# Kernel tuning notes

Hardware: AMD Instinct MI355X
Metric: run time of the kernel (lower is better)

Reference implementation:

```python
import jax, jax.numpy as jnp
import numpy as np

EMBED_DIM = 1024
NUM_HEADS = 16
HEAD_DIM = EMBED_DIM // NUM_HEADS


def setup_inputs() -> dict:
    key = jax.random.key(0)
    ks = jax.random.split(key, 9)
    B, S, D = 2, 2048, EMBED_DIM
    scale = 1.0 / np.sqrt(D)
    x = jax.random.normal(ks[0], (B, S, D), dtype=jnp.float32)
    wq = jax.random.normal(ks[1], (D, D), dtype=jnp.float32) * scale
    bq = jax.random.normal(ks[2], (D,), dtype=jnp.float32) * 0.02
    wk = jax.random.normal(ks[3], (D, D), dtype=jnp.float32) * scale
    bk = jax.random.normal(ks[4], (D,), dtype=jnp.float32) * 0.02
    wv = jax.random.normal(ks[5], (D, D), dtype=jnp.float32) * scale
    bv = jax.random.normal(ks[6], (D,), dtype=jnp.float32) * 0.02
    wo = jax.random.normal(ks[7], (D, D), dtype=jnp.float32) * scale
    bo = jax.random.normal(ks[8], (D,), dtype=jnp.float32) * 0.02
    return {"x": x, "wq": wq, "bq": bq, "wk": wk, "bk": bk,
            "wv": wv, "bv": bv, "wo": wo, "bo": bo}


def reference(x, wq, bq, wk, bk, wv, bv, wo, bo):
    B, S, D = x.shape
    H, Hd = NUM_HEADS, HEAD_DIM
    # separate QKV linears (weights stored [in, out] so x @ w)
    q = (x @ wq + bq).reshape(B, S, H, Hd).transpose(0, 2, 1, 3)  # [B,H,S,Hd]
    k = (x @ wk + bk).reshape(B, S, H, Hd).transpose(0, 2, 1, 3)
    v = (x @ wv + bv).reshape(B, S, H, Hd).transpose(0, 2, 1, 3)
    scores = jnp.einsum('bhqd,bhkd->bhqk', q, k) / jnp.sqrt(jnp.float32(Hd))
    attn = jax.nn.softmax(scores, axis=-1)
    context = jnp.einsum('bhqk,bhkd->bhqd', attn, v)
    context = context.transpose(0, 2, 1, 3).reshape(B, S, D)
    return context @ wo + bo
```

## Files before the change

kernel.cpp:

```cpp
#include <hip/hip_runtime.h>
#include <cstdint>
#include <cstddef>


typedef float floatx4 __attribute__((ext_vector_type(4)));
typedef __bf16 bf16x8 __attribute__((ext_vector_type(8)));
union ABFrag { bf16x8 v; uint4 q; unsigned short u[8]; unsigned int w[4]; };

__device__ __forceinline__ unsigned short f2bf(float f) {
    unsigned int u = __builtin_bit_cast(unsigned int, f);
    return (unsigned short)((u + 0x7FFFu + ((u >> 16) & 1u)) >> 16);
}

__device__ __forceinline__ unsigned int pkbf(float lo, float hi) {
    unsigned int a = __builtin_bit_cast(unsigned int, hi) + 0x8000u;
    unsigned int b = __builtin_bit_cast(unsigned int, lo) + 0x8000u;
    return __builtin_amdgcn_perm(a, b, 0x07060302u);
}

#if __has_builtin(__builtin_amdgcn_exp2f)
#define EXP2F(x) __builtin_amdgcn_exp2f(x)
#else
#define EXP2F(x) exp2f(x)
#endif

__device__ __forceinline__ void glds16(const void* g, void* l) {
    __builtin_amdgcn_global_load_lds(
        (const __attribute__((address_space(1))) unsigned int*)(uintptr_t)g,
        (__attribute__((address_space(3))) unsigned int*)(unsigned int)(uintptr_t)l,
        16, 0, 0);
}

__global__ void convert_x_kernel(const float* __restrict__ x,
                                 unsigned short* __restrict__ xb) {
    int i = (blockIdx.x * 256 + threadIdx.x) * 8;
    float4 a = *(const float4*)(x + i);
    float4 b = *(const float4*)(x + i + 4);
    union { unsigned short u[8]; uint4 q; } o;
    o.u[0] = f2bf(a.x); o.u[1] = f2bf(a.y); o.u[2] = f2bf(a.z); o.u[3] = f2bf(a.w);
    o.u[4] = f2bf(b.x); o.u[5] = f2bf(b.y); o.u[6] = f2bf(b.z); o.u[7] = f2bf(b.w);
    *(uint4*)(xb + i) = o.q;
}

__global__ void convert_wT_kernel(const float* __restrict__ w0, const float* __restrict__ w1,
                                  const float* __restrict__ w2, const float* __restrict__ w3,
                                  unsigned short* __restrict__ wT) {
    __shared__ unsigned short t[32][40];
    const float* w = (blockIdx.z == 0) ? w0 : (blockIdx.z == 1) ? w1
                   : (blockIdx.z == 2) ? w2 : w3;
    unsigned short* dst = wT + (size_t)blockIdx.z * 1024 * 1024;
    const int k0 = blockIdx.x * 32, n0 = blockIdx.y * 32;
    const int tid = threadIdx.x;
    {
        int ry = tid >> 3, cx = (tid & 7) * 4;
        float4 v = *(const float4*)(w + (size_t)(k0 + ry) * 1024 + n0 + cx);
        t[cx + 0][ry] = f2bf(v.x); t[cx + 1][ry] = f2bf(v.y);
        t[cx + 2][ry] = f2bf(v.z); t[cx + 3][ry] = f2bf(v.w);
    }
    __syncthreads();
    int n = tid >> 3, kc = (tid & 7) * 4;
    *(uint2*)(dst + (size_t)(n0 + n) * 1024 + k0 + kc) = *(const uint2*)&t[n][kc];
}

template<int KIND>
__launch_bounds__(256, 2)
__global__ void gemm_kernel(const unsigned short* __restrict__ A,
                            const unsigned short* __restrict__ wT,
                            const float* __restrict__ bias0,
                            const float* __restrict__ bias1,
                            const float* __restrict__ bias2,
                            void* __restrict__ out0,
                            void* __restrict__ out1,
                            void* __restrict__ out2)
{
    constexpr int BN = (KIND == 1) ? 64 : 128;
    constexpr int NJ = BN / 32;

    __shared__ unsigned short a_s[128 * 32];
    __shared__ unsigned short b_s[BN * 32];

    const int tid  = threadIdx.x;
    const int wid  = tid >> 6;
    const int lane = tid & 63;
    const int quad = lane >> 4;
    const int l15  = lane & 15;
    const int wm   = (wid >> 1) * 64;
    const int wn   = (wid & 1) * (BN / 2);
    const int m0   = blockIdx.y * 128;
    const int n0   = blockIdx.x * BN;

    const unsigned short* Bt = (KIND == 0) ? wT + (size_t)blockIdx.z * (1024 * 1024) : wT;
    const float* bias = (KIND == 0)
        ? (blockIdx.z == 0 ? bias0 : blockIdx.z == 1 ? bias1 : bias2) : bias0;

    const int sr = lane >> 2;
    const int sc = (lane & 3) * 8;
    const unsigned short* gA = A + (size_t)(m0 + wid * 32 + sr) * 1024 + sc;
    const unsigned short* gB = (KIND == 0)
        ? Bt + (size_t)(n0 + wid * 32 + sr) * 1024 + sc
        : Bt + (size_t)(n0 + wid * 16 + sr) * 1024 + sc;
    unsigned short* lA = a_s + wid * 1024;
    unsigned short* lB = (KIND == 0) ? b_s + wid * 1024 : b_s + wid * 512;

    floatx4 acc[4][NJ];
    #pragma unroll
    for (int i = 0; i < 4; i++)
        #pragma unroll
        for (int j = 0; j < NJ; j++)
            acc[i][j] = floatx4{0.f, 0.f, 0.f, 0.f};

    for (int k0 = 0; k0 < 1024; k0 += 32) {
        __syncthreads();
        glds16(gA + k0,             lA);
        glds16(gA + k0 + 16 * 1024, lA + 512);
        if constexpr (KIND == 0) {
            glds16(gB + k0,             lB);
            glds16(gB + k0 + 16 * 1024, lB + 512);
        } else {
            glds16(gB + k0,             lB);
        }
        __syncthreads();

        ABFrag af[4], bf4[NJ];
        #pragma unroll
        for (int i = 0; i < 4; i++)
            af[i].q = *(const uint4*)(a_s + (wm + i * 16 + l15) * 32 + quad * 8);
        #pragma unroll
        for (int j = 0; j < NJ; j++)
            bf4[j].q = *(const uint4*)(b_s + (wn + j * 16 + l15) * 32 + quad * 8);
        #pragma unroll
        for (int i = 0; i < 4; i++)
            #pragma unroll
            for (int j = 0; j < NJ; j++)
                acc[i][j] = __builtin_amdgcn_mfma_f32_16x16x32_bf16(
                    af[i].v, bf4[j].v, acc[i][j], 0, 0, 0);
    }

    if constexpr (KIND == 1) {
        float* out = (float*)out0;
        #pragma unroll
        for (int j = 0; j < NJ; j++) {
            int gn = n0 + wn + j * 16 + l15;
            float bval = bias[gn];
            #pragma unroll
            for (int i = 0; i < 4; i++)
                #pragma unroll
                for (int r = 0; r < 4; r++) {
                    int gm = m0 + wm + i * 16 + quad * 4 + r;
                    out[(size_t)gm * 1024 + gn] = acc[i][j][r] + bval;
                }
        }
    } else {
        if (blockIdx.z == 0) {
            const float SCQ = 0.125f * 1.44269504088896f;
            unsigned short* out = (unsigned short*)out0;
            #pragma unroll
            for (int j = 0; j < 4; j++) {
                int gn = n0 + wn + j * 16 + l15;
                float bval = bias[gn];
                int h = gn >> 6, d = gn & 63;
                #pragma unroll
                for (int i = 0; i < 4; i++)
                    #pragma unroll
                    for (int r = 0; r < 4; r++) {
                        int gm = m0 + wm + i * 16 + quad * 4 + r;
                        int b = gm >> 11, s = gm & 2047;
                        out[(((size_t)(b * 16 + h) * 2048 + s) << 6) + d] =
                            f2bf((acc[i][j][r] + bval) * SCQ);
                    }
            }
        } else if (blockIdx.z == 1) {
            unsigned short* out = (unsigned short*)out1;
            #pragma unroll
            for (int j = 0; j < 4; j++) {
                int gn = n0 + wn + j * 16 + l15;
                float bval = bias[gn];
                int h = gn >> 6, d = gn & 63;
                int dg = d >> 3, dl = d & 7;
                #pragma unroll
                for (int i = 0; i < 4; i++)
                    #pragma unroll
                    for (int r = 0; r < 4; r++) {
                        int gm = m0 + wm + i * 16 + quad * 4 + r;
                        int b = gm >> 11, s = gm & 2047;
                        int dphys = ((dg ^ (s & 7)) << 3) | dl;
                        out[(((size_t)(b * 16 + h) * 2048 + s) << 6) + dphys] =
                            f2bf(acc[i][j][r] + bval);
                    }
            }
        } else {
            __shared__ unsigned short t_s[128][136];
            #pragma unroll
            for (int j = 0; j < 4; j++) {
                int nl = wn + j * 16 + l15;
                float bval = bias[n0 + nl];
                #pragma unroll
                for (int i = 0; i < 4; i++)
                    #pragma unroll
                    for (int r = 0; r < 4; r++)
                        t_s[nl][wm + i * 16 + quad * 4 + r] = f2bf(acc[i][j][r] + bval);
            }
            __syncthreads();
            unsigned short* out = (unsigned short*)out2;
            const int n  = tid >> 1, half = tid & 1;
            const int bh = (m0 >> 11) * 16 + ((n0 + n) >> 6);
            const int d  = (n0 + n) & 63;
            const int chunk = ((m0 & 2047) >> 6) + half;
            const int dmask = d & 7;
            unsigned short* dstb = out + ((size_t)(bh * 32 + chunk) * 64 + d) * 64;
            const unsigned short* src = &t_s[n][half * 64];
            #pragma unroll
            for (int gp = 0; gp < 8; gp++) {
                int u1 = 32 * (gp >> 2) + 4 * (gp & 3);
                uint2 lo = *(const uint2*)(src + u1);
                uint2 hi = *(const uint2*)(src + u1 + 16);
                unsigned short* dq = dstb + ((gp ^ dmask) << 3);
                *(uint2*)dq       = lo;
                *(uint2*)(dq + 4) = hi;
            }
        }
    }
}

__launch_bounds__(512, 4)
__global__ void attn_kernel(const unsigned short* __restrict__ Q,
                            const unsigned short* __restrict__ K,
                            const unsigned short* __restrict__ Vt,
                            unsigned short* __restrict__ ctx)
{
    __shared__ unsigned short smem[2][2][2][4096];

    const int tid  = threadIdx.x;
    const int wid  = tid >> 6;
    const int kh   = wid >> 2;
    const int wq   = wid & 3;
    const int lane = tid & 63;
    const int quad = lane >> 4;
    const int l15  = lane & 15;
    const int xr   = l15 & 7;

    const int bh = blockIdx.y;
    const unsigned short* Qh = Q + (size_t)bh * (2048 * 64);
    const char* Kc = (const char*)(K  + (size_t)bh * (2048 * 64)) + (size_t)kh * (16 * 8192);
    const char* Vc = (const char*)(Vt + (size_t)bh * (2048 * 64)) + (size_t)kh * (16 * 8192);
    const int q0 = blockIdx.x * 128 + wq * 32;

    ABFrag qf[2][2];
    #pragma unroll
    for (int jq = 0; jq < 2; jq++)
        #pragma unroll
        for (int s = 0; s < 2; s++)
            qf[jq][s].q = *(const uint4*)(Qh + (size_t)(q0 + jq * 16 + l15) * 64
                                          + s * 32 + quad * 8);

    int kcol[2];
    kcol[0] = ((quad    ) ^ xr) << 3;
    kcol[1] = ((quad + 4) ^ xr) << 3;

    floatx4 acc[4][2];
    #pragma unroll
    for (int i = 0; i < 4; i++)
        #pragma unroll
        for (int jq = 0; jq < 2; jq++)
            acc[i][jq] = floatx4{0.f, 0.f, 0.f, 0.f};
    float lrun[2] = {0.f, 0.f};

    auto stage = [&](int c, int b) {
        const char* gk = Kc + (size_t)c * 8192 + wq * 2048 + lane * 16;
        char* lk = (char*)&smem[b][kh][0][0] + wq * 2048;
        glds16(gk,        lk);
        glds16(gk + 1024, lk + 1024);
        const char* gv = Vc + (size_t)c * 8192 + wq * 2048 + lane * 16;
        char* lv = (char*)&smem[b][kh][1][0] + wq * 2048;
        glds16(gv,        lv);
        glds16(gv + 1024, lv + 1024);
    };

    stage(0, 0);

    for (int c = 0; c < 16; ++c) {
        const int b = c & 1;
        __syncthreads();
        if (c + 1 < 16) stage(c + 1, b ^ 1);

        const unsigned short* ks = &smem[b][kh][0][0];
        const unsigned short* vs = &smem[b][kh][1][0];

        floatx4 st[4][2];
        __builtin_amdgcn_s_setprio(1);
        #pragma unroll
        for (int kt = 0; kt < 4; kt++) {
            ABFrag k0, k1;
            const unsigned short* kr = ks + (kt * 16 + l15) * 64;
            k0.q = *(const uint4*)(kr + kcol[0]);
            k1.q = *(const uint4*)(kr + kcol[1]);
            #pragma unroll
            for (int jq = 0; jq < 2; jq++) {
                floatx4 t = floatx4{0.f, 0.f, 0.f, 0.f};
                t = __builtin_amdgcn_mfma_f32_16x16x32_bf16(k0.v, qf[jq][0].v, t, 0, 0, 0);
                t = __builtin_amdgcn_mfma_f32_16x16x32_bf16(k1.v, qf[jq][1].v, t, 0, 0, 0);
                st[kt][jq] = t;
            }
        }
        __builtin_amdgcn_s_setprio(0);

        unsigned int pk[4][2][2];
        #pragma unroll
        for (int jq = 0; jq < 2; jq++) {
            float ls = 0.f;
            #pragma unroll
            for (int kt = 0; kt < 4; kt++) {
                #pragma unroll
                for (int t2 = 0; t2 < 2; t2++) {
                    float p0 = EXP2F(st[kt][jq][2 * t2 + 0]);
                    float p1 = EXP2F(st[kt][jq][2 * t2 + 1]);
                    ls += p0 + p1;
                    pk[kt][jq][t2] = pkbf(p0, p1);
                }
            }
            lrun[jq] += ls;
        }

        __builtin_amdgcn_s_setprio(1);
        #pragma unroll
        for (int s2 = 0; s2 < 2; s2++) {
            ABFrag pf[2];
            #pragma unroll
            for (int jq = 0; jq < 2; jq++) {
                pf[jq].w[0] = pk[2 * s2 + 0][jq][0];
                pf[jq].w[1] = pk[2 * s2 + 0][jq][1];
                pf[jq].w[2] = pk[2 * s2 + 1][jq][0];
                pf[jq].w[3] = pk[2 * s2 + 1][jq][1];
            }
            #pragma unroll
            for (int i = 0; i < 4; i++) {
                ABFrag vf;
                vf.q = *(const uint4*)(vs + (i * 16 + l15) * 64 + kcol[s2]);
                #pragma unroll
                for (int jq = 0; jq < 2; jq++)
                    acc[i][jq] = __builtin_amdgcn_mfma_f32_16x16x32_bf16(
                        vf.v, pf[jq].v, acc[i][jq], 0, 0, 0);
            }
        }
        __builtin_amdgcn_s_setprio(0);
    }

    __syncthreads();
    float* sf = (float*)&smem[0][0][0][0];
    float* myp = sf + (size_t)(wq * 64 + lane) * 40;
    if (kh) {
        #pragma unroll
        for (int i = 0; i < 4; i++)
            #pragma unroll
            for (int jq = 0; jq < 2; jq++)
                *(floatx4*)(myp + (i * 2 + jq) * 4) = acc[i][jq];
        myp[32] = lrun[0];
        myp[33] = lrun[1];
    }
    __syncthreads();
    if (!kh) {
        #pragma unroll
        for (int i = 0; i < 4; i++)
            #pragma unroll
            for (int jq = 0; jq < 2; jq++)
                acc[i][jq] += *(const floatx4*)(myp + (i * 2 + jq) * 4);
        lrun[0] += myp[32];
        lrun[1] += myp[33];

        const int b_ = bh >> 4, h = bh & 15;
        #pragma unroll
        for (int jq = 0; jq < 2; jq++) {
            float s = lrun[jq];
            s += __shfl_xor(s, 16, 64);
            s += __shfl_xor(s, 32, 64);
            float inv = 1.0f / s;
            int q = q0 + jq * 16 + l15;
            size_t base = (size_t)(b_ * 2048 + q) * 1024 + h * 64;
            #pragma unroll
            for (int i = 0; i < 4; i++) {
                float v0 = acc[i][jq][0] * inv, v1 = acc[i][jq][1] * inv;
                float v2 = acc[i][jq][2] * inv, v3 = acc[i][jq][3] * inv;
                uint2 w2 = make_uint2(pkbf(v0, v1), pkbf(v2, v3));
                *(uint2*)(ctx + base + i * 16 + quad * 4) = w2;
            }
        }
    }
}

extern "C" void kernel_launch(void* const* d_in, const int* in_sizes, int n_in,
                              void* d_out, int out_size, void* d_ws, size_t ws_size,
                              hipStream_t stream)
{
    const float* x  = (const float*)d_in[0];
    const float* wq = (const float*)d_in[1];
    const float* bq = (const float*)d_in[2];
    const float* wk = (const float*)d_in[3];
    const float* bk = (const float*)d_in[4];
    const float* wv = (const float*)d_in[5];
    const float* bv = (const float*)d_in[6];
    const float* wo = (const float*)d_in[7];
    const float* bo = (const float*)d_in[8];

    const size_t NE = (size_t)4096 * 1024;
    unsigned short* xb  = (unsigned short*)d_ws;
    unsigned short* wT  = xb  + NE;
    unsigned short* qb  = wT  + NE;
    unsigned short* kb  = qb  + NE;
    unsigned short* vtb = kb  + NE;
    unsigned short* ctx = vtb + NE;

    hipLaunchKernelGGL(convert_x_kernel, dim3(2048), dim3(256), 0, stream, x, xb);
    hipLaunchKernelGGL(convert_wT_kernel, dim3(32, 32, 4), dim3(256), 0, stream,
                       wq, wk, wv, wo, wT);
    hipLaunchKernelGGL((gemm_kernel<0>), dim3(8, 32, 3), dim3(256), 0, stream,
                       xb, wT, bq, bk, bv, (void*)qb, (void*)kb, (void*)vtb);
    hipLaunchKernelGGL(attn_kernel, dim3(16, 32), dim3(512), 0, stream, qb, kb, vtb, ctx);
    hipLaunchKernelGGL((gemm_kernel<1>), dim3(16, 32), dim3(256), 0, stream,
                       ctx, wT + 3 * NE / 4, bo, nullptr, nullptr, d_out, nullptr, nullptr);
}
```

Before: 186.9 us.

## Fuse conversion kernels, shrink output GEMM tile, use hardware bf16 pack, drop setprio

Merges the x conversion and the weight transpose/convert into one launch, which removes one kernel launch gap. Shrinks the output-projection GEMM tile to 64x64 so the grid has twice as many blocks for better CU occupancy, at the cost of less reuse per block. Replaces the manual round-and-permute bf16 packing with the v_cvt_pk_bf16_f32 instruction in the attention kernel, and removes the s_setprio hints around the MFMA sections.

```diff
diff --git a/kernel.cpp b/kernel.cpp
--- a/kernel.cpp
+++ b/kernel.cpp
@@ -12,10 +12,10 @@
     return (unsigned short)((u + 0x7FFFu + ((u >> 16) & 1u)) >> 16);
 }
 
-__device__ __forceinline__ unsigned int pkbf(float lo, float hi) {
-    unsigned int a = __builtin_bit_cast(unsigned int, hi) + 0x8000u;
-    unsigned int b = __builtin_bit_cast(unsigned int, lo) + 0x8000u;
-    return __builtin_amdgcn_perm(a, b, 0x07060302u);
+__device__ __forceinline__ unsigned int cvtpk(float lo, float hi) {
+    unsigned int r;
+    asm("v_cvt_pk_bf16_f32 %0, %1, %2" : "=v"(r) : "v"(lo), "v"(hi));
+    return r;
 }
 
 #if __has_builtin(__builtin_amdgcn_exp2f)
@@ -31,26 +31,31 @@
         16, 0, 0);
 }
 
-__global__ void convert_x_kernel(const float* __restrict__ x,
-                                 unsigned short* __restrict__ xb) {
-    int i = (blockIdx.x * 256 + threadIdx.x) * 8;
-    float4 a = *(const float4*)(x + i);
-    float4 b = *(const float4*)(x + i + 4);
-    union { unsigned short u[8]; uint4 q; } o;
-    o.u[0] = f2bf(a.x); o.u[1] = f2bf(a.y); o.u[2] = f2bf(a.z); o.u[3] = f2bf(a.w);
-    o.u[4] = f2bf(b.x); o.u[5] = f2bf(b.y); o.u[6] = f2bf(b.z); o.u[7] = f2bf(b.w);
-    *(uint4*)(xb + i) = o.q;
-}
-
-__global__ void convert_wT_kernel(const float* __restrict__ w0, const float* __restrict__ w1,
-                                  const float* __restrict__ w2, const float* __restrict__ w3,
-                                  unsigned short* __restrict__ wT) {
+__global__ void convert_fused_kernel(const float* __restrict__ x,
+                                     const float* __restrict__ w0,
+                                     const float* __restrict__ w1,
+                                     const float* __restrict__ w2,
+                                     const float* __restrict__ w3,
+                                     unsigned short* __restrict__ xb,
+                                     unsigned short* __restrict__ wT) {
+    const int tid = threadIdx.x;
+    if (blockIdx.x < 2048) {
+        int i = (blockIdx.x * 256 + tid) * 8;
+        float4 a = *(const float4*)(x + i);
+        float4 b = *(const float4*)(x + i + 4);
+        union { unsigned short u[8]; uint4 q; } o;
+        o.u[0] = f2bf(a.x); o.u[1] = f2bf(a.y); o.u[2] = f2bf(a.z); o.u[3] = f2bf(a.w);
+        o.u[4] = f2bf(b.x); o.u[5] = f2bf(b.y); o.u[6] = f2bf(b.z); o.u[7] = f2bf(b.w);
+        *(uint4*)(xb + i) = o.q;
+        return;
+    }
     __shared__ unsigned short t[32][40];
-    const float* w = (blockIdx.z == 0) ? w0 : (blockIdx.z == 1) ? w1
-                   : (blockIdx.z == 2) ? w2 : w3;
-    unsigned short* dst = wT + (size_t)blockIdx.z * 1024 * 1024;
-    const int k0 = blockIdx.x * 32, n0 = blockIdx.y * 32;
-    const int tid = threadIdx.x;
+    const int wi = blockIdx.x - 2048;
+    const int z  = wi >> 10;
+    const int rem = wi & 1023;
+    const int k0 = (rem >> 5) * 32, n0 = (rem & 31) * 32;
+    const float* w = (z == 0) ? w0 : (z == 1) ? w1 : (z == 2) ? w2 : w3;
+    unsigned short* dst = wT + (size_t)z * 1024 * 1024;
     {
         int ry = tid >> 3, cx = (tid & 7) * 4;
         float4 v = *(const float4*)(w + (size_t)(k0 + ry) * 1024 + n0 + cx);
@@ -73,10 +78,12 @@
                             void* __restrict__ out1,
                             void* __restrict__ out2)
 {
+    constexpr int BM = (KIND == 1) ? 64 : 128;
     constexpr int BN = (KIND == 1) ? 64 : 128;
+    constexpr int NI = BM / 32;
     constexpr int NJ = BN / 32;
 
-    __shared__ unsigned short a_s[128 * 32];
+    __shared__ unsigned short a_s[BM * 32];
     __shared__ unsigned short b_s[BN * 32];
 
     const int tid  = threadIdx.x;
@@ -84,9 +91,9 @@
     const int lane = tid & 63;
     const int quad = lane >> 4;
     const int l15  = lane & 15;
-    const int wm   = (wid >> 1) * 64;
+    const int wm   = (wid >> 1) * (BM / 2);
     const int wn   = (wid & 1) * (BN / 2);
-    const int m0   = blockIdx.y * 128;
+    const int m0   = blockIdx.y * BM;
     const int n0   = blockIdx.x * BN;
 
     const unsigned short* Bt = (KIND == 0) ? wT + (size_t)blockIdx.z * (1024 * 1024) : wT;
@@ -95,41 +102,35 @@
 
     const int sr = lane >> 2;
     const int sc = (lane & 3) * 8;
-    const unsigned short* gA = A + (size_t)(m0 + wid * 32 + sr) * 1024 + sc;
-    const unsigned short* gB = (KIND == 0)
-        ? Bt + (size_t)(n0 + wid * 32 + sr) * 1024 + sc
-        : Bt + (size_t)(n0 + wid * 16 + sr) * 1024 + sc;
-    unsigned short* lA = a_s + wid * 1024;
-    unsigned short* lB = (KIND == 0) ? b_s + wid * 1024 : b_s + wid * 512;
-
-    floatx4 acc[4][NJ];
+    const unsigned short* gA = A + (size_t)(m0 + wid * (BM / 4) + sr) * 1024 + sc;
+    const unsigned short* gB = Bt + (size_t)(n0 + wid * (BN / 4) + sr) * 1024 + sc;
+    unsigned short* lA = a_s + wid * (BM / 4) * 32;
+    unsigned short* lB = b_s + wid * (BN / 4) * 32;
+
+    floatx4 acc[NI][NJ];
     #pragma unroll
-    for (int i = 0; i < 4; i++)
+    for (int i = 0; i < NI; i++)
         #pragma unroll
         for (int j = 0; j < NJ; j++)
             acc[i][j] = floatx4{0.f, 0.f, 0.f, 0.f};
 
     for (int k0 = 0; k0 < 1024; k0 += 32) {
         __syncthreads();
-        glds16(gA + k0,             lA);
-        glds16(gA + k0 + 16 * 1024, lA + 512);
-        if constexpr (KIND == 0) {
-            glds16(gB + k0,             lB);
-            glds16(gB + k0 + 16 * 1024, lB + 512);
-        } else {
-            glds16(gB + k0,             lB);
-        }
+        glds16(gA + k0, lA);
+        if constexpr (KIND == 0) glds16(gA + k0 + 16 * 1024, lA + 512);
+        glds16(gB + k0, lB);
+        if constexpr (KIND == 0) glds16(gB + k0 + 16 * 1024, lB + 512);
         __syncthreads();
 
-        ABFrag af[4], bf4[NJ];
-        #pragma unroll
-        for (int i = 0; i < 4; i++)
+        ABFrag af[NI], bf4[NJ];
+        #pragma unroll
+        for (int i = 0; i < NI; i++)
             af[i].q = *(const uint4*)(a_s + (wm + i * 16 + l15) * 32 + quad * 8);
         #pragma unroll
         for (int j = 0; j < NJ; j++)
             bf4[j].q = *(const uint4*)(b_s + (wn + j * 16 + l15) * 32 + quad * 8);
         #pragma unroll
-        for (int i = 0; i < 4; i++)
+        for (int i = 0; i < NI; i++)
             #pragma unroll
             for (int j = 0; j < NJ; j++)
                 acc[i][j] = __builtin_amdgcn_mfma_f32_16x16x32_bf16(
@@ -143,7 +144,7 @@
             int gn = n0 + wn + j * 16 + l15;
             float bval = bias[gn];
             #pragma unroll
-            for (int i = 0; i < 4; i++)
+            for (int i = 0; i < NI; i++)
                 #pragma unroll
                 for (int r = 0; r < 4; r++) {
                     int gm = m0 + wm + i * 16 + quad * 4 + r;
@@ -287,7 +288,6 @@
         const unsigned short* vs = &smem[b][kh][1][0];
 
         floatx4 st[4][2];
-        __builtin_amdgcn_s_setprio(1);
         #pragma unroll
         for (int kt = 0; kt < 4; kt++) {
             ABFrag k0, k1;
@@ -302,7 +302,6 @@
                 st[kt][jq] = t;
             }
         }
-        __builtin_amdgcn_s_setprio(0);
 
         unsigned int pk[4][2][2];
         #pragma unroll
@@ -315,13 +314,12 @@
                     float p0 = EXP2F(st[kt][jq][2 * t2 + 0]);
                     float p1 = EXP2F(st[kt][jq][2 * t2 + 1]);
                     ls += p0 + p1;
-                    pk[kt][jq][t2] = pkbf(p0, p1);
+                    pk[kt][jq][t2] = cvtpk(p0, p1);
                 }
             }
             lrun[jq] += ls;
         }
 
-        __builtin_amdgcn_s_setprio(1);
         #pragma unroll
         for (int s2 = 0; s2 < 2; s2++) {
             ABFrag pf[2];
@@ -342,7 +340,6 @@
                         vf.v, pf[jq].v, acc[i][jq], 0, 0, 0);
             }
         }
-        __builtin_amdgcn_s_setprio(0);
     }
 
     __syncthreads();
@@ -380,7 +377,7 @@
             for (int i = 0; i < 4; i++) {
                 float v0 = acc[i][jq][0] * inv, v1 = acc[i][jq][1] * inv;
                 float v2 = acc[i][jq][2] * inv, v3 = acc[i][jq][3] * inv;
-                uint2 w2 = make_uint2(pkbf(v0, v1), pkbf(v2, v3));
+                uint2 w2 = make_uint2(cvtpk(v0, v1), cvtpk(v2, v3));
                 *(uint2*)(ctx + base + i * 16 + quad * 4) = w2;
             }
         }
@@ -409,12 +406,11 @@
     unsigned short* vtb = kb  + NE;
     unsigned short* ctx = vtb + NE;
 
-    hipLaunchKernelGGL(convert_x_kernel, dim3(2048), dim3(256), 0, stream, x, xb);
-    hipLaunchKernelGGL(convert_wT_kernel, dim3(32, 32, 4), dim3(256), 0, stream,
-                       wq, wk, wv, wo, wT);
+    hipLaunchKernelGGL(convert_fused_kernel, dim3(6144), dim3(256), 0, stream,
+                       x, wq, wk, wv, wo, xb, wT);
     hipLaunchKernelGGL((gemm_kernel<0>), dim3(8, 32, 3), dim3(256), 0, stream,
                        xb, wT, bq, bk, bv, (void*)qb, (void*)kb, (void*)vtb);
     hipLaunchKernelGGL(attn_kernel, dim3(16, 32), dim3(512), 0, stream, qb, kb, vtb, ctx);
-    hipLaunchKernelGGL((gemm_kernel<1>), dim3(16, 32), dim3(256), 0, stream,
+    hipLaunchKernelGGL((gemm_kernel<1>), dim3(16, 64), dim3(256), 0, stream,
                        ctx, wT + 3 * NE / 4, bo, nullptr, nullptr, d_out, nullptr, nullptr);
 }
```

Measured after the change: 184.6 us. About the same (-1.3%).
